# Optimization experiments

Hardware: AMD Instinct MI355X
Metric: run time of the kernel (lower is better)

The kernel has to match this reference:

```python
import jax, jax.numpy as jnp
import numpy as np
from jax import lax

N, M, B = 512, 1024, 1024  # signal dim, atoms, batch (batch==m required by X = W @ Gamma)
POWER_ITER = 100
IHT_ITER = 50


def setup_inputs() -> dict:
    key = jax.random.key(0)
    k1, k2 = jax.random.split(key)
    Y = jax.random.normal(k1, (B, N), dtype=jnp.float32)
    W = jax.random.normal(k2, (N, M), dtype=jnp.float32)
    return {"Y": Y, "W": W, "K": 64}


def power_method(W):
    # 100 iterations of X <- X W^T W / ||.||; returns last pre-normalization norm
    # (approx largest eigenvalue of W^T W), matching PowerMethod in the source.
    X0 = jax.random.normal(jax.random.key(42), (1, W.shape[1]), dtype=W.dtype)

    def body(i, carry):
        X, _ = carry
        X2 = (X @ W.T) @ W          # [1, m]
        nm = jnp.linalg.norm(X2)
        return (X2 / nm, nm)

    _, nm = lax.fori_loop(0, POWER_ITER, body, (X0, jnp.asarray(1.0, W.dtype)))
    return nm


def hard_threshold_k(G, K):
    # keep entries strictly larger (in abs) than the (K+1)-th largest per row
    a = jnp.sort(jnp.abs(G), axis=1)[:, ::-1]   # descending per row
    T = a[:, K][:, None]                          # [B, 1]
    return G * (jnp.abs(G) > T).astype(G.dtype)


def reference(Y, W, K):
    # NormDict: column-normalize the dictionary
    W = W / jnp.linalg.norm(W, axis=0)
    c = power_method(W)
    eta = 1.0 / c
    Yn = jnp.linalg.norm(Y)

    # IHT sparse coding
    Gamma = hard_threshold_k(Y @ (eta * W), K)     # [B, m]
    residual = Gamma @ W.T - Y                      # [B, n]

    def step(carry, _):
        Gamma, residual = carry
        Gamma = hard_threshold_k(Gamma - eta * (residual @ W), K)
        residual = Gamma @ W.T - Y
        return (Gamma, residual), jnp.linalg.norm(residual) / Yn

    (Gamma, residual), norms = lax.scan(step, (Gamma, residual), None, length=IHT_ITER)

    X = W @ Gamma  # [n, m] @ [B, m] -> requires B == m, as in the torch source
    return X, Gamma, norms
```

## Files before the change

### kernel.cpp

```cpp
#include <hip/hip_runtime.h>


#define DEV __device__ __forceinline__

constexpr int Nd = 512;
constexpr int Md = 1024;
constexpr int Bd = 1024;
constexpr int Ksp = 64;
constexpr int IHT = 50;

DEV float wave_reduce_f(float v) {
#pragma unroll
  for (int off = 32; off > 0; off >>= 1) v += __shfl_down(v, off);
  return v;
}
DEV double wave_reduce_d(double v) {
#pragma unroll
  for (int off = 32; off > 0; off >>= 1) v += __shfl_down(v, off);
  return v;
}
DEV float rfl_f(float v) {
  return __uint_as_float(__builtin_amdgcn_readfirstlane(__float_as_uint(v)));
}

__global__ __launch_bounds__(256) void k_colnorm(const float* __restrict__ W,
                                                 float* __restrict__ cnorm,
                                                 double* __restrict__ dacc) {
  if (blockIdx.x == 0 && threadIdx.x < 51) dacc[threadIdx.x] = 0.0;
  int col = blockIdx.x * 256 + threadIdx.x;
  double ss = 0.0;
  for (int i = 0; i < Nd; ++i) {
    float w = W[(size_t)i * Md + col];
    ss = fma((double)w, (double)w, ss);
  }
  cnorm[col] = (float)sqrt(ss);
}

__global__ __launch_bounds__(256) void k_normalize(const float* __restrict__ W,
                                                   const float* __restrict__ cnorm,
                                                   float* __restrict__ Wn) {
  int idx = blockIdx.x * 256 + threadIdx.x;
  Wn[idx] = W[idx] / cnorm[idx & (Md - 1)];
}

__global__ __launch_bounds__(256) void k_yn2(const float* __restrict__ Y,
                                             double* __restrict__ dacc) {
  double s = 0.0;
  for (int i = blockIdx.x * 256 + threadIdx.x; i < Bd * Nd; i += gridDim.x * 256) {
    float y = Y[i];
    s = fma((double)y, (double)y, s);
  }
  s = wave_reduce_d(s);
  __shared__ double red[4];
  int lane = threadIdx.x & 63, wid = threadIdx.x >> 6;
  if (lane == 0) red[wid] = s;
  __syncthreads();
  if (threadIdx.x == 0) atomicAdd(&dacc[0], red[0] + red[1] + red[2] + red[3]);
}

template <int BM, int BN, int TN>
__global__ __launch_bounds__(256) void k_gemm_t(const float* __restrict__ A, int lda, int ta,
                                                const float* __restrict__ B, int ldb, int tb,
                                                float* __restrict__ C, int ldc, int Kd,
                                                float scale) {
  constexpr int AE = 32 * BM / 256;
  constexpr int BE = 32 * BN / 256;
  __shared__ __align__(16) float As[32][BM + 4];
  __shared__ __align__(16) float Bs[32][BN + 4];
  const int tid = threadIdx.x;
  const int tx = tid % (BN / TN), ty = tid / (BN / TN);
  const int m0 = blockIdx.y * BM, n0 = blockIdx.x * BN;
  float ra[AE], rb[BE];
  float acc[4][TN];
#pragma unroll
  for (int i = 0; i < 4; ++i)
#pragma unroll
    for (int j = 0; j < TN; ++j) acc[i][j] = 0.f;

  auto loadA = [&](int k0) {
    if (!ta) {
      const int c = tid & 31, r0 = tid >> 5;
#pragma unroll
      for (int i = 0; i < AE; ++i)
        ra[i] = A[(size_t)(m0 + r0 + i * 8) * lda + (k0 + c)];
    } else {
      const int r = tid % BM, c0 = tid / BM;
#pragma unroll
      for (int i = 0; i < AE; ++i)
        ra[i] = A[(size_t)(k0 + c0 + i * (256 / BM)) * lda + (m0 + r)];
    }
  };
  auto storeA = [&]() {
    if (!ta) {
      const int c = tid & 31, r0 = tid >> 5;
#pragma unroll
      for (int i = 0; i < AE; ++i) As[c][r0 + i * 8] = ra[i];
    } else {
      const int r = tid % BM, c0 = tid / BM;
#pragma unroll
      for (int i = 0; i < AE; ++i) As[c0 + i * (256 / BM)][r] = ra[i];
    }
  };
  auto loadB = [&](int k0) {
    if (!tb) {
      const int c = tid % BN, r0 = tid / BN;
#pragma unroll
      for (int i = 0; i < BE; ++i)
        rb[i] = B[(size_t)(k0 + r0 + i * (256 / BN)) * ldb + (n0 + c)];
    } else {
      const int r = tid & 31, c0 = tid >> 5;
#pragma unroll
      for (int i = 0; i < BE; ++i)
        rb[i] = B[(size_t)(n0 + c0 + i * 8) * ldb + (k0 + r)];
    }
  };
  auto storeB = [&]() {
    if (!tb) {
      const int c = tid % BN, r0 = tid / BN;
#pragma unroll
      for (int i = 0; i < BE; ++i) Bs[r0 + i * (256 / BN)][c] = rb[i];
    } else {
      const int r = tid & 31, c0 = tid >> 5;
#pragma unroll
      for (int i = 0; i < BE; ++i) Bs[r][c0 + i * 8] = rb[i];
    }
  };

  loadA(0);
  loadB(0);
  storeA();
  storeB();
  __syncthreads();
  for (int k0 = 0; k0 < Kd; k0 += 32) {
    const bool more = (k0 + 32) < Kd;
    if (more) { loadA(k0 + 32); loadB(k0 + 32); }
#pragma unroll
    for (int kk = 0; kk < 32; ++kk) {
      const float4 a4 = *(const float4*)&As[kk][ty * 4];
      const float aa[4] = {a4.x, a4.y, a4.z, a4.w};
      float bb[TN];
      if constexpr (TN == 4) {
        const float4 b4 = *(const float4*)&Bs[kk][tx * 4];
        bb[0] = b4.x; bb[1] = b4.y; bb[2] = b4.z; bb[3] = b4.w;
      } else {
        const float2 b2 = *(const float2*)&Bs[kk][tx * 2];
        bb[0] = b2.x; bb[1] = b2.y;
      }
#pragma unroll
      for (int i = 0; i < 4; ++i)
#pragma unroll
        for (int j = 0; j < TN; ++j) acc[i][j] = fmaf(aa[i], bb[j], acc[i][j]);
    }
    if (more) {
      __syncthreads();
      storeA();
      storeB();
      __syncthreads();
    }
  }
#pragma unroll
  for (int i = 0; i < 4; ++i) {
    if constexpr (TN == 4) {
      float4 o;
      o.x = acc[i][0] * scale; o.y = acc[i][1] * scale;
      o.z = acc[i][2] * scale; o.w = acc[i][3] * scale;
      *(float4*)&C[(size_t)(m0 + ty * 4 + i) * ldc + n0 + tx * 4] = o;
    } else {
      float2 o;
      o.x = acc[i][0] * scale; o.y = acc[i][1] * scale;
      *(float2*)&C[(size_t)(m0 + ty * 4 + i) * ldc + n0 + tx * 2] = o;
    }
  }
}

DEV float erfinv_xla(float x) {
  float w = -log1pf(-x * x);
  float p;
  if (w < 5.0f) {
    w = w - 2.5f;
    p = 2.81022636e-08f;
    p = fmaf(p, w, 3.43273939e-07f);
    p = fmaf(p, w, -3.5233877e-06f);
    p = fmaf(p, w, -4.39150654e-06f);
    p = fmaf(p, w, 0.00021858087f);
    p = fmaf(p, w, -0.00125372503f);
    p = fmaf(p, w, -0.00417768164f);
    p = fmaf(p, w, 0.246640727f);
    p = fmaf(p, w, 1.50140941f);
  } else {
    w = sqrtf(w) - 3.0f;
    p = -0.000200214257f;
    p = fmaf(p, w, 0.000100950558f);
    p = fmaf(p, w, 0.00134934322f);
    p = fmaf(p, w, -0.00367342844f);
    p = fmaf(p, w, 0.00573950773f);
    p = fmaf(p, w, -0.0076224613f);
    p = fmaf(p, w, 0.00943887047f);
    p = fmaf(p, w, 1.00167406f);
    p = fmaf(p, w, 2.83297682f);
  }
  return p * x;
}

#define TF_ROUND(r)                                  \
  {                                                  \
    x0 += x1;                                        \
    x1 = (x1 << (r)) | (x1 >> (32 - (r)));           \
    x1 ^= x0;                                        \
  }

DEV float x0_value(unsigned i, int hi) {
  unsigned x0 = i, x1 = i + 512u;
  const unsigned ks0 = 0u, ks1 = 42u, ks2 = 0x1BD11BDAu ^ 42u;
  x0 += ks0; x1 += ks1;
  TF_ROUND(13) TF_ROUND(15) TF_ROUND(26) TF_ROUND(6)  x0 += ks1; x1 += ks2 + 1u;
  TF_ROUND(17) TF_ROUND(29) TF_ROUND(16) TF_ROUND(24) x0 += ks2; x1 += ks0 + 2u;
  TF_ROUND(13) TF_ROUND(15) TF_ROUND(26) TF_ROUND(6)  x0 += ks0; x1 += ks1 + 3u;
  TF_ROUND(17) TF_ROUND(29) TF_ROUND(16) TF_ROUND(24) x0 += ks1; x1 += ks2 + 4u;
  TF_ROUND(13) TF_ROUND(15) TF_ROUND(26) TF_ROUND(6)  x0 += ks2; x1 += ks0 + 5u;
  const float lo = -0.99999994f;
  const float sqrt2 = 1.41421356237f;
  const unsigned bits = hi ? x1 : x0;
  float f = __uint_as_float((bits >> 9) | 0x3f800000u) - 1.0f;
  float u = fmaxf(lo, f * 2.0f + lo);
  return sqrt2 * erfinv_xla(u);
}

__global__ __launch_bounds__(256) void k_z0(const float* __restrict__ Wn,
                                            float* __restrict__ vout) {
  __shared__ float x0s[Md];
  const int t = threadIdx.x;
  x0s[t] = x0_value((unsigned)t, 0);
  x0s[t + 512] = x0_value((unsigned)t, 1);
  x0s[t + 256] = x0_value((unsigned)(t + 256), 0);
  x0s[t + 768] = x0_value((unsigned)(t + 256), 1);
  __syncthreads();
  const int lane = t & 63, wid = t >> 6;
  const int row = blockIdx.x * 4 + wid;
  const float4* wr = (const float4*)(Wn + (size_t)row * Md);
  const float4* x4 = (const float4*)x0s;
  float s = 0.f;
#pragma unroll
  for (int e = 0; e < 4; ++e) {
    const float4 w4 = wr[lane + e * 64];
    const float4 xx = x4[lane + e * 64];
    s = fmaf(w4.x, xx.x, s); s = fmaf(w4.y, xx.y, s);
    s = fmaf(w4.z, xx.z, s); s = fmaf(w4.w, xx.w, s);
  }
  s = wave_reduce_f(s);
  if (lane == 0) vout[row] = s;
}

__global__ __launch_bounds__(256) void k_pmv(const float* __restrict__ Mmat,
                                             const float* __restrict__ vin,
                                             float* __restrict__ vout, float scale) {
  const int lane = threadIdx.x & 63, wid = threadIdx.x >> 6;
  const int row = blockIdx.x * 4 + wid;
  const float4* mr = (const float4*)(Mmat + (size_t)row * Nd);
  const float4* v4 = (const float4*)vin;
  float s = 0.f;
#pragma unroll
  for (int e = 0; e < 2; ++e) {
    const float4 m4 = mr[lane + e * 64];
    const float4 xx = v4[lane + e * 64];
    s = fmaf(m4.x, xx.x, s); s = fmaf(m4.y, xx.y, s);
    s = fmaf(m4.z, xx.z, s); s = fmaf(m4.w, xx.w, s);
  }
  s = wave_reduce_f(s);
  if (lane == 0) vout[row] = s * scale;
}

__global__ __launch_bounds__(512) void k_pfinal(const float* __restrict__ v99,
                                                const float* __restrict__ v100,
                                                float* __restrict__ cbuf) {
  __shared__ double r99[8], r100[8];
  const int t = threadIdx.x, lane = t & 63, wid = t >> 6;
  double a = (double)v99[t]; a *= a;
  double b = (double)v100[t]; b *= b;
  a = wave_reduce_d(a);
  b = wave_reduce_d(b);
  if (lane == 0) { r99[wid] = a; r100[wid] = b; }
  __syncthreads();
  if (t == 0) {
    double n99 = 0.0, n100 = 0.0;
    for (int i = 0; i < 8; ++i) { n99 += r99[i]; n100 += r100[i]; }
    float c = (float)(8.0 * sqrt(n100 / n99));
    cbuf[0] = c;
    cbuf[1] = 1.0f / c;
  }
}

__global__ __launch_bounds__(256, 4) void k_iht_all(
    const float* __restrict__ Q, const float* __restrict__ YW,
    const float* __restrict__ cbuf, float* __restrict__ gdense,
    double* __restrict__ normacc) {
  __shared__ float u[Md];
  __shared__ float yws[Md];
  __shared__ float sval[Ksp];
  __shared__ int sidx[Ksp];
  __shared__ unsigned histbuf[2][4][256];
  __shared__ unsigned wred[4];
  __shared__ unsigned sel_need, sel_prefix;
  __shared__ double dred0;
  __shared__ int scnt;

  const int t = threadIdx.x;
  const int b = blockIdx.x;
  const int lane = t & 63, wv = t >> 6;
  const float eta = cbuf[1];
  const float4 yw = ((const float4*)(YW + (size_t)b * Md))[t];
  ((float4*)yws)[t] = yw;
#pragma unroll
  for (int e = 0; e < 8; ++e) ((unsigned*)histbuf)[t + e * 256] = 0u;
  const float* Qt = Q + t * 4;
  float gdr[4] = {0.f, 0.f, 0.f, 0.f};

  auto scan_select = [&](unsigned(*hist)[256], unsigned pfx, unsigned nd, int sh) {
    const unsigned c0 = hist[0][lane] + hist[1][lane] + hist[2][lane] + hist[3][lane];
    const unsigned c1 = hist[0][lane + 64] + hist[1][lane + 64] + hist[2][lane + 64] + hist[3][lane + 64];
    const unsigned c2 = hist[0][lane + 128] + hist[1][lane + 128] + hist[2][lane + 128] + hist[3][lane + 128];
    const unsigned c3 = hist[0][lane + 192] + hist[1][lane + 192] + hist[2][lane + 192] + hist[3][lane + 192];
    unsigned s0 = c0, s1 = c1, s2 = c2, s3 = c3;
#pragma unroll
    for (int off = 1; off < 64; off <<= 1) {
      const unsigned y0 = __shfl_down(s0, off), y1 = __shfl_down(s1, off);
      const unsigned y2 = __shfl_down(s2, off), y3 = __shfl_down(s3, off);
      if (lane + off < 64) { s0 += y0; s1 += y1; s2 += y2; s3 += y3; }
    }
    const unsigned T1 = __builtin_amdgcn_readfirstlane(s1);
    const unsigned T2 = __builtin_amdgcn_readfirstlane(s2);
    const unsigned T3 = __builtin_amdgcn_readfirstlane(s3);
    const unsigned i0 = s0 + T1 + T2 + T3;
    const unsigned i1 = s1 + T2 + T3;
    const unsigned i2 = s2 + T3;
    const unsigned i3 = s3;
    if (i0 >= nd && i0 - c0 < nd) { sel_prefix = pfx | ((unsigned)lane << sh); sel_need = nd - (i0 - c0); }
    if (i1 >= nd && i1 - c1 < nd) { sel_prefix = pfx | ((unsigned)(lane + 64) << sh); sel_need = nd - (i1 - c1); }
    if (i2 >= nd && i2 - c2 < nd) { sel_prefix = pfx | ((unsigned)(lane + 128) << sh); sel_need = nd - (i2 - c2); }
    if (i3 >= nd && i3 - c3 < nd) { sel_prefix = pfx | ((unsigned)(lane + 192) << sh); sel_need = nd - (i3 - c3); }
  };

  for (int it = -1; it < IHT; ++it) {
    float vals[4];
    unsigned key[4];
    int cnt = 0;
    if (it >= 0) {
      cnt = scnt;
      float4 p = make_float4(0.f, 0.f, 0.f, 0.f);
      float4 qa[8], qb[8];
      float ga[8], gb[8];
      auto LOAD8 = [&](float4* q, float* g, int kk) {
#pragma unroll
        for (int j = 0; j < 8; ++j) {
          const int id = __builtin_amdgcn_readfirstlane(sidx[kk + j]);
          g[j] = rfl_f(sval[kk + j]);
          q[j] = *(const float4*)(Qt + (size_t)id * Md);
        }
      };
      auto FMA8 = [&](const float4* q, const float* g) {
#pragma unroll
        for (int j = 0; j < 8; ++j) p.x = fmaf(g[j], q[j].x, p.x);
#pragma unroll
        for (int j = 0; j < 8; ++j) p.y = fmaf(g[j], q[j].y, p.y);
#pragma unroll
        for (int j = 0; j < 8; ++j) p.z = fmaf(g[j], q[j].z, p.z);
#pragma unroll
        for (int j = 0; j < 8; ++j) p.w = fmaf(g[j], q[j].w, p.w);
      };
      int k = 0;
      const int nfull = cnt & ~7;
      if (nfull >= 8) {
        LOAD8(qa, ga, 0);
        k = 8;
        for (; k + 16 <= nfull; k += 16) {
          LOAD8(qb, gb, k);
          FMA8(qa, ga);
          LOAD8(qa, ga, k + 8);
          FMA8(qb, gb);
        }
        if (k + 8 <= nfull) {
          LOAD8(qb, gb, k);
          FMA8(qa, ga);
          FMA8(qb, gb);
          k += 8;
        } else {
          FMA8(qa, ga);
        }
      }
      for (; k < cnt; ++k) {
        const int id = __builtin_amdgcn_readfirstlane(sidx[k]);
        const float g = rfl_f(sval[k]);
        const float4 q = *(const float4*)(Qt + (size_t)id * Md);
        p.x = fmaf(g, q.x, p.x); p.y = fmaf(g, q.y, p.y);
        p.z = fmaf(g, q.z, p.z); p.w = fmaf(g, q.w, p.w);
      }
      ((float4*)u)[t] = p;
      vals[0] = -(eta * (p.x - yw.x)) + gdr[0];
      vals[1] = -(eta * (p.y - yw.y)) + gdr[1];
      vals[2] = -(eta * (p.z - yw.z)) + gdr[2];
      vals[3] = -(eta * (p.w - yw.w)) + gdr[3];
    } else {
      vals[0] = eta * yw.x; vals[1] = eta * yw.y;
      vals[2] = eta * yw.z; vals[3] = eta * yw.w;
      __syncthreads();
    }
#pragma unroll
    for (int e = 0; e < 4; ++e) key[e] = __float_as_uint(vals[e]) & 0x7fffffffu;

#pragma unroll
    for (int e = 0; e < 4; ++e) atomicAdd(&histbuf[1][wv][key[e] >> 24], 1u);
    __syncthreads();
    if (wv == 0) {
      scan_select(histbuf[1], 0u, Ksp + 1, 24);
    } else if (wv == 1) {
      if (it >= 1) {
        double part = 0.0;
        if (lane < cnt) {
          const int id = sidx[lane];
          part = (double)sval[lane] * ((double)u[id] - 2.0 * (double)yws[id]);
        }
        part = wave_reduce_d(part);
        if (lane == 0) dred0 = part;
      }
    } else {
      unsigned* hz = (unsigned*)histbuf[0] + (wv - 2) * 512;
#pragma unroll
      for (int e = 0; e < 8; ++e) hz[lane + e * 64] = 0u;
    }
    __syncthreads();
    unsigned prefix = sel_prefix;
    unsigned need = sel_need;
    unsigned pmask = 0xFF000000u;

#pragma unroll
    for (int pass = 2; pass >= 0; --pass) {
      const int sh = 8 * pass;
      const int pb = pass & 1;
      unsigned(*hist)[256] = histbuf[pb];
#pragma unroll
      for (int e = 0; e < 4; ++e)
        if ((key[e] & pmask) == prefix) atomicAdd(&hist[wv][(key[e] >> sh) & 255u], 1u);
      if (pass == 2 && it >= 1 && t == 0) atomicAdd(&normacc[it - 1], dred0);
      __syncthreads();
      unsigned* hz = histbuf[pb ^ 1][wv];
      hz[lane] = 0u; hz[lane + 64] = 0u; hz[lane + 128] = 0u; hz[lane + 192] = 0u;
      if (wv == 0) scan_select(hist, prefix, need, sh);
      __syncthreads();
      prefix = sel_prefix;
      need = sel_need;
      pmask |= (255u << sh);
    }
    const unsigned Tbits = prefix;

    unsigned keep = 0u;
    unsigned myc = 0u;
#pragma unroll
    for (int e = 0; e < 4; ++e)
      if (key[e] > Tbits) { keep |= (1u << e); ++myc; }
    gdr[0] = (keep & 1u) ? vals[0] : 0.f;
    gdr[1] = (keep & 2u) ? vals[1] : 0.f;
    gdr[2] = (keep & 4u) ? vals[2] : 0.f;
    gdr[3] = (keep & 8u) ? vals[3] : 0.f;
    unsigned x = myc;
#pragma unroll
    for (int off = 1; off < 64; off <<= 1) {
      const unsigned y = __shfl_up(x, off);
      if (lane >= off) x += y;
    }
    if (lane == 63) wred[wv] = x;
    __syncthreads();
    unsigned addlo = 0u;
    for (int w2 = 0; w2 < wv; ++w2) addlo += wred[w2];
    int base = (int)(x + addlo) - (int)myc;
#pragma unroll
    for (int e = 0; e < 4; ++e) {
      if (keep & (1u << e)) {
        sidx[base] = t * 4 + e;
        sval[base] = vals[e];
        ++base;
      }
    }
    if (t == 0) scnt = (int)(wred[0] + wred[1] + wred[2] + wred[3]);
    if (it == IHT - 1) {
      float4 g;
      g.x = gdr[0]; g.y = gdr[1]; g.z = gdr[2]; g.w = gdr[3];
      ((float4*)(gdense + (size_t)b * Md))[t] = g;
    }
    __syncthreads();
  }

  const int cnt = scnt;
  if (wv == 0) {
    double part = 0.0;
    if (lane < cnt) {
      const int id = sidx[lane];
      float acc2 = 0.f;
      for (int k = 0; k < cnt; ++k)
        acc2 = fmaf(sval[k], Q[(size_t)sidx[k] * Md + id], acc2);
      part = (double)sval[lane] * ((double)acc2 - 2.0 * (double)yws[id]);
    }
    part = wave_reduce_d(part);
    if (lane == 0) atomicAdd(&normacc[IHT - 1], part);
  }
}

__global__ void k_wnorms(const double* __restrict__ dacc, float* __restrict__ onorms) {
  const int t = threadIdx.x;
  if (t < IHT) {
    const double yn2 = dacc[0];
    double r2 = yn2 + dacc[1 + t];
    if (r2 < 0.0) r2 = 0.0;
    onorms[t] = (float)(sqrt(r2) / sqrt(yn2));
  }
}

extern "C" void kernel_launch(void* const* d_in, const int* in_sizes, int n_in,
                              void* d_out, int out_size, void* d_ws, size_t ws_size,
                              hipStream_t stream) {
  (void)in_sizes; (void)n_in; (void)out_size; (void)ws_size;
  const float* Y = (const float*)d_in[0];
  const float* W = (const float*)d_in[1];
  float* out = (float*)d_out;
  float* outX = out;
  float* outG = out + Nd * Md;
  float* outN = outG + Bd * Md;

  char* wsb = (char*)d_ws;
  double* dacc = (double*)wsb;
  float* cbuf = (float*)(wsb + 512);
  float* Wn = (float*)(wsb + 1024);
  float* Q = Wn + Nd * Md;
  float* YW = Q + Md * Md;
  float* Smat = YW + Bd * Md;
  float* S2 = Smat + Nd * Nd;
  float* cnorm = S2 + Nd * Nd;
  float* X0 = cnorm + Md;
  float* V = X0 + Md;

  k_colnorm<<<4, 256, 0, stream>>>(W, cnorm, dacc);
  k_normalize<<<2048, 256, 0, stream>>>(W, cnorm, Wn);

  k_gemm_t<64, 32, 2><<<dim3(16, 8), 256, 0, stream>>>(Wn, Md, 0, Wn, Md, 1, Smat, Nd, Md, 1.0f);
  k_gemm_t<64, 32, 2><<<dim3(16, 8), 256, 0, stream>>>(Smat, Nd, 0, Smat, Nd, 0, S2, Nd, Nd, 0.015625f);
  k_gemm_t<64, 64, 4><<<dim3(16, 16), 256, 0, stream>>>(Wn, Md, 1, Wn, Md, 0, Q, Md, Nd, 1.0f);
  k_gemm_t<64, 64, 4><<<dim3(16, 16), 256, 0, stream>>>(Y, Nd, 0, Wn, Md, 0, YW, Md, Nd, 1.0f);
  k_yn2<<<128, 256, 0, stream>>>(Y, dacc);

  k_z0<<<128, 256, 0, stream>>>(Wn, V);
  float* pin = V;
  float* pout = V + 512;
  for (int i = 0; i < 49; ++i) {
    k_pmv<<<128, 256, 0, stream>>>(S2, pin, pout, 1.0f);
    float* tp = pin; pin = pout; pout = tp;
  }
  k_pmv<<<128, 256, 0, stream>>>(Smat, pin, V + 1024, 0.125f);
  k_pmv<<<128, 256, 0, stream>>>(Smat, V + 1024, V + 1536, 0.125f);
  k_pfinal<<<1, 512, 0, stream>>>(V + 1024, V + 1536, cbuf);

  k_iht_all<<<1024, 256, 0, stream>>>(Q, YW, cbuf, outG, dacc + 1);
  k_wnorms<<<1, 64, 0, stream>>>(dacc, outN);

  k_gemm_t<64, 32, 2><<<dim3(32, 8), 256, 0, stream>>>(Wn, Md, 0, outG, Md, 0, outX, Md, Md, 1.0f);
}
```

Baseline: 938.4 us.

## Merge independent front-end GEMMs and reductions into one multi-role kernel launch

Folds three independent GEMMs (W^T W, Wn^T Wn, Y Wn), the ||Y||^2 reduction and the power-method start vector into a single kernel that dispatches on block index. The final X GEMM is merged with the norms-output kernel the same way. Shared memory becomes one flat buffer passed to a device-function GEMM. This removes five launches and lets independent work share one wave of the GPU. In exchange, heterogeneous blocks can unbalance the schedule, and the larger shared allocation may lower occupancy for the smaller-tile GEMM.

```diff
diff --git a/kernel.cpp b/kernel.cpp
--- a/kernel.cpp
+++ b/kernel.cpp
@@ -43,33 +43,19 @@
   Wn[idx] = W[idx] / cnorm[idx & (Md - 1)];
 }
 
-__global__ __launch_bounds__(256) void k_yn2(const float* __restrict__ Y,
-                                             double* __restrict__ dacc) {
-  double s = 0.0;
-  for (int i = blockIdx.x * 256 + threadIdx.x; i < Bd * Nd; i += gridDim.x * 256) {
-    float y = Y[i];
-    s = fma((double)y, (double)y, s);
-  }
-  s = wave_reduce_d(s);
-  __shared__ double red[4];
-  int lane = threadIdx.x & 63, wid = threadIdx.x >> 6;
-  if (lane == 0) red[wid] = s;
-  __syncthreads();
-  if (threadIdx.x == 0) atomicAdd(&dacc[0], red[0] + red[1] + red[2] + red[3]);
-}
-
 template <int BM, int BN, int TN>
-__global__ __launch_bounds__(256) void k_gemm_t(const float* __restrict__ A, int lda, int ta,
-                                                const float* __restrict__ B, int ldb, int tb,
-                                                float* __restrict__ C, int ldc, int Kd,
-                                                float scale) {
+DEV void gemm_dev(float* __restrict__ AsB, float* __restrict__ BsB,
+                  const float* __restrict__ A, int lda, int ta,
+                  const float* __restrict__ B, int ldb, int tb,
+                  float* __restrict__ C, int ldc, int Kd, float scale,
+                  int bx, int by) {
   constexpr int AE = 32 * BM / 256;
   constexpr int BE = 32 * BN / 256;
-  __shared__ __align__(16) float As[32][BM + 4];
-  __shared__ __align__(16) float Bs[32][BN + 4];
+  constexpr int AS = BM + 4;
+  constexpr int BS = BN + 4;
   const int tid = threadIdx.x;
   const int tx = tid % (BN / TN), ty = tid / (BN / TN);
-  const int m0 = blockIdx.y * BM, n0 = blockIdx.x * BN;
+  const int m0 = by * BM, n0 = bx * BN;
   float ra[AE], rb[BE];
   float acc[4][TN];
 #pragma unroll
@@ -94,11 +80,11 @@
     if (!ta) {
       const int c = tid & 31, r0 = tid >> 5;
 #pragma unroll
-      for (int i = 0; i < AE; ++i) As[c][r0 + i * 8] = ra[i];
+      for (int i = 0; i < AE; ++i) AsB[c * AS + r0 + i * 8] = ra[i];
     } else {
       const int r = tid % BM, c0 = tid / BM;
 #pragma unroll
-      for (int i = 0; i < AE; ++i) As[c0 + i * (256 / BM)][r] = ra[i];
+      for (int i = 0; i < AE; ++i) AsB[(c0 + i * (256 / BM)) * AS + r] = ra[i];
     }
   };
   auto loadB = [&](int k0) {
@@ -118,11 +104,11 @@
     if (!tb) {
       const int c = tid % BN, r0 = tid / BN;
 #pragma unroll
-      for (int i = 0; i < BE; ++i) Bs[r0 + i * (256 / BN)][c] = rb[i];
+      for (int i = 0; i < BE; ++i) BsB[(r0 + i * (256 / BN)) * BS + c] = rb[i];
     } else {
       const int r = tid & 31, c0 = tid >> 5;
 #pragma unroll
-      for (int i = 0; i < BE; ++i) Bs[r][c0 + i * 8] = rb[i];
+      for (int i = 0; i < BE; ++i) BsB[r * BS + c0 + i * 8] = rb[i];
     }
   };
 
@@ -136,14 +122,14 @@
     if (more) { loadA(k0 + 32); loadB(k0 + 32); }
 #pragma unroll
     for (int kk = 0; kk < 32; ++kk) {
-      const float4 a4 = *(const float4*)&As[kk][ty * 4];
+      const float4 a4 = *(const float4*)&AsB[kk * AS + ty * 4];
       const float aa[4] = {a4.x, a4.y, a4.z, a4.w};
       float bb[TN];
       if constexpr (TN == 4) {
-        const float4 b4 = *(const float4*)&Bs[kk][tx * 4];
+        const float4 b4 = *(const float4*)&BsB[kk * BS + tx * 4];
         bb[0] = b4.x; bb[1] = b4.y; bb[2] = b4.z; bb[3] = b4.w;
       } else {
-        const float2 b2 = *(const float2*)&Bs[kk][tx * 2];
+        const float2 b2 = *(const float2*)&BsB[kk * BS + tx * 2];
         bb[0] = b2.x; bb[1] = b2.y;
       }
 #pragma unroll
@@ -171,6 +157,16 @@
       *(float2*)&C[(size_t)(m0 + ty * 4 + i) * ldc + n0 + tx * 2] = o;
     }
   }
+}
+
+template <int BM, int BN, int TN>
+__global__ __launch_bounds__(256) void k_gemm_t(const float* __restrict__ A, int lda, int ta,
+                                                const float* __restrict__ B, int ldb, int tb,
+                                                float* __restrict__ C, int ldc, int Kd,
+                                                float scale) {
+  __shared__ __align__(16) float smem[32 * (BM + 4) + 32 * (BN + 4)];
+  gemm_dev<BM, BN, TN>(smem, smem + 32 * (BM + 4), A, lda, ta, B, ldb, tb, C,
+                       ldc, Kd, scale, blockIdx.x, blockIdx.y);
 }
 
 DEV float erfinv_xla(float x) {
@@ -226,29 +222,60 @@
   return sqrt2 * erfinv_xla(u);
 }
 
-__global__ __launch_bounds__(256) void k_z0(const float* __restrict__ Wn,
-                                            float* __restrict__ vout) {
-  __shared__ float x0s[Md];
+__global__ __launch_bounds__(256) void k_front(
+    const float* __restrict__ Wn, const float* __restrict__ Y,
+    float* __restrict__ Smat, float* __restrict__ Qm, float* __restrict__ YWm,
+    double* __restrict__ dacc, float* __restrict__ vout) {
+  __shared__ __align__(16) float smem[4352];
+  const int i = blockIdx.x;
   const int t = threadIdx.x;
-  x0s[t] = x0_value((unsigned)t, 0);
-  x0s[t + 512] = x0_value((unsigned)t, 1);
-  x0s[t + 256] = x0_value((unsigned)(t + 256), 0);
-  x0s[t + 768] = x0_value((unsigned)(t + 256), 1);
-  __syncthreads();
-  const int lane = t & 63, wid = t >> 6;
-  const int row = blockIdx.x * 4 + wid;
-  const float4* wr = (const float4*)(Wn + (size_t)row * Md);
-  const float4* x4 = (const float4*)x0s;
-  float s = 0.f;
-#pragma unroll
-  for (int e = 0; e < 4; ++e) {
-    const float4 w4 = wr[lane + e * 64];
-    const float4 xx = x4[lane + e * 64];
-    s = fmaf(w4.x, xx.x, s); s = fmaf(w4.y, xx.y, s);
-    s = fmaf(w4.z, xx.z, s); s = fmaf(w4.w, xx.w, s);
-  }
-  s = wave_reduce_f(s);
-  if (lane == 0) vout[row] = s;
+  if (i < 128) {
+    gemm_dev<64, 32, 2>(smem, smem + 32 * 68, Wn, Md, 0, Wn, Md, 1, Smat, Nd,
+                        Md, 1.0f, i % 16, i / 16);
+  } else if (i < 384) {
+    const int j = i - 128;
+    gemm_dev<64, 64, 4>(smem, smem + 32 * 68, Wn, Md, 1, Wn, Md, 0, Qm, Md,
+                        Nd, 1.0f, j % 16, j / 16);
+  } else if (i < 640) {
+    const int j = i - 384;
+    gemm_dev<64, 64, 4>(smem, smem + 32 * 68, Y, Nd, 0, Wn, Md, 0, YWm, Md,
+                        Nd, 1.0f, j % 16, j / 16);
+  } else if (i < 768) {
+    const int j = i - 640;
+    double* red = (double*)smem;
+    double s = 0.0;
+    for (int idx = j * 256 + t; idx < Bd * Nd; idx += 128 * 256) {
+      float y = Y[idx];
+      s = fma((double)y, (double)y, s);
+    }
+    s = wave_reduce_d(s);
+    const int lane = t & 63, wid = t >> 6;
+    if (lane == 0) red[wid] = s;
+    __syncthreads();
+    if (t == 0) atomicAdd(&dacc[0], red[0] + red[1] + red[2] + red[3]);
+  } else {
+    const int j = i - 768;
+    float* x0s = smem;
+    x0s[t] = x0_value((unsigned)t, 0);
+    x0s[t + 512] = x0_value((unsigned)t, 1);
+    x0s[t + 256] = x0_value((unsigned)(t + 256), 0);
+    x0s[t + 768] = x0_value((unsigned)(t + 256), 1);
+    __syncthreads();
+    const int lane = t & 63, wid = t >> 6;
+    const int row = j * 4 + wid;
+    const float4* wr = (const float4*)(Wn + (size_t)row * Md);
+    const float4* x4 = (const float4*)x0s;
+    float s = 0.f;
+#pragma unroll
+    for (int e = 0; e < 4; ++e) {
+      const float4 w4 = wr[lane + e * 64];
+      const float4 xx = x4[lane + e * 64];
+      s = fmaf(w4.x, xx.x, s); s = fmaf(w4.y, xx.y, s);
+      s = fmaf(w4.z, xx.z, s); s = fmaf(w4.w, xx.w, s);
+    }
+    s = wave_reduce_f(s);
+    if (lane == 0) vout[row] = s;
+  }
 }
 
 __global__ __launch_bounds__(256) void k_pmv(const float* __restrict__ Mmat,
@@ -504,13 +531,23 @@
   }
 }
 
-__global__ void k_wnorms(const double* __restrict__ dacc, float* __restrict__ onorms) {
-  const int t = threadIdx.x;
-  if (t < IHT) {
-    const double yn2 = dacc[0];
-    double r2 = yn2 + dacc[1 + t];
-    if (r2 < 0.0) r2 = 0.0;
-    onorms[t] = (float)(sqrt(r2) / sqrt(yn2));
+__global__ __launch_bounds__(256) void k_back(
+    const float* __restrict__ Wn, const float* __restrict__ G,
+    float* __restrict__ X, const double* __restrict__ dacc,
+    float* __restrict__ onorms) {
+  __shared__ __align__(16) float smem[4352];
+  const int i = blockIdx.x;
+  if (i < 256) {
+    gemm_dev<64, 32, 2>(smem, smem + 32 * 68, Wn, Md, 0, G, Md, 0, X, Md, Md,
+                        1.0f, i % 32, i / 32);
+  } else {
+    const int t = threadIdx.x;
+    if (t < IHT) {
+      const double yn2 = dacc[0];
+      double r2 = yn2 + dacc[1 + t];
+      if (r2 < 0.0) r2 = 0.0;
+      onorms[t] = (float)(sqrt(r2) / sqrt(yn2));
+    }
   }
 }
 
@@ -540,13 +577,10 @@
   k_colnorm<<<4, 256, 0, stream>>>(W, cnorm, dacc);
   k_normalize<<<2048, 256, 0, stream>>>(W, cnorm, Wn);
 
-  k_gemm_t<64, 32, 2><<<dim3(16, 8), 256, 0, stream>>>(Wn, Md, 0, Wn, Md, 1, Smat, Nd, Md, 1.0f);
+  k_front<<<896, 256, 0, stream>>>(Wn, Y, Smat, Q, YW, dacc, V);
+
   k_gemm_t<64, 32, 2><<<dim3(16, 8), 256, 0, stream>>>(Smat, Nd, 0, Smat, Nd, 0, S2, Nd, Nd, 0.015625f);
-  k_gemm_t<64, 64, 4><<<dim3(16, 16), 256, 0, stream>>>(Wn, Md, 1, Wn, Md, 0, Q, Md, Nd, 1.0f);
-  k_gemm_t<64, 64, 4><<<dim3(16, 16), 256, 0, stream>>>(Y, Nd, 0, Wn, Md, 0, YW, Md, Nd, 1.0f);
-  k_yn2<<<128, 256, 0, stream>>>(Y, dacc);
-
-  k_z0<<<128, 256, 0, stream>>>(Wn, V);
+
   float* pin = V;
   float* pout = V + 512;
   for (int i = 0; i < 49; ++i) {
@@ -558,7 +592,6 @@
   k_pfinal<<<1, 512, 0, stream>>>(V + 1024, V + 1536, cbuf);
 
   k_iht_all<<<1024, 256, 0, stream>>>(Q, YW, cbuf, outG, dacc + 1);
-  k_wnorms<<<1, 64, 0, stream>>>(dacc, outN);
-
-  k_gemm_t<64, 32, 2><<<dim3(32, 8), 256, 0, stream>>>(Wn, Md, 0, outG, Md, 0, outX, Md, Md, 1.0f);
-}
+
+  k_back<<<257, 256, 0, stream>>>(Wn, outG, outX, dacc, outN);
+}
```

Result: faster. 878.1 us, median of 2 (-6.4%).
